# Kernel tuning notes

Hardware: AMD Instinct MI355X
Metric: run time of the kernel (lower is better)

The kernel has to match this reference:

```python
import jax, jax.numpy as jnp
import numpy as np

D_MODEL = 1024
BATCH = 4
SEQ = 4096


def setup_inputs() -> dict:
    key = jax.random.key(0)
    kx, kwz, kwh = jax.random.split(key, 3)
    scale = 1.0 / np.sqrt(D_MODEL)
    x = jax.random.normal(kx, (BATCH, SEQ, D_MODEL), dtype=jnp.float32)
    Wz = jax.random.normal(kwz, (D_MODEL, D_MODEL), dtype=jnp.float32) * scale
    bz = jnp.zeros((D_MODEL,), dtype=jnp.float32)
    Wh = jax.random.normal(kwh, (D_MODEL, D_MODEL), dtype=jnp.float32) * scale
    bh = jnp.zeros((D_MODEL,), dtype=jnp.float32)
    return {"x": x, "Wz": Wz, "bz": bz, "Wh": Wh, "bh": bh}


def _parallel_scan_real(a, b):
    # h_t = a_t * h_{t-1} + b_t via log-depth associative scan along time axis.
    def binary_op(left, right):
        a_l, b_l = left
        a_r, b_r = right
        return (a_l * a_r, a_r * b_l + b_r)
    _, h = jax.lax.associative_scan(binary_op, (a, b), axis=1)
    return h


def reference(x, Wz, bz, Wh, bh):
    # x: [B, T, D]
    z = jax.nn.sigmoid(jnp.einsum('btd,de->bte', x, Wz) + bz)  # update gate
    h_tilde = jnp.einsum('btd,de->bte', x, Wh) + bh            # candidate
    return _parallel_scan_real(1.0 - z, z * h_tilde)           # [B, T, D]
```

## Files before the change

kernel.cpp:

```cpp
#include <hip/hip_runtime.h>
#include <hip/hip_bf16.h>
#include <stdint.h>

#define D_MODEL 1024
#define BATCH   4
#define SEQ     4096
#define M_TOTAL (BATCH*SEQ)
#define KDIM    D_MODEL

#define NC 128
#define CL (SEQ/NC)

#define BM 128
#define BN 128
#define BK 32

typedef __bf16 bf16x8 __attribute__((ext_vector_type(8)));
typedef float  f32x4  __attribute__((ext_vector_type(4)));

static __device__ __forceinline__ unsigned short f2bf(float f) {
  unsigned u = __builtin_bit_cast(unsigned, f);
  u += 0x7FFFu + ((u >> 16) & 1u);
  return (unsigned short)(u >> 16);
}

__global__ __launch_bounds__(256) void k_cvt_x(const float* __restrict__ x,
                                               unsigned short* __restrict__ xb) {
  int i = blockIdx.x * 256 + threadIdx.x;
  float4 v = ((const float4*)x)[i];
  ushort4 o;
  o.x = f2bf(v.x); o.y = f2bf(v.y); o.z = f2bf(v.z); o.w = f2bf(v.w);
  ((ushort4*)xb)[i] = o;
}

__global__ void k_cvt_wT(const float* __restrict__ Wz, const float* __restrict__ Wh,
                         unsigned short* __restrict__ WzT, unsigned short* __restrict__ WhT) {
  __shared__ float tile[32][33];
  const float* W = blockIdx.z ? Wh : Wz;
  unsigned short* O = blockIdx.z ? WhT : WzT;
  int bx = blockIdx.x * 32;
  int by = blockIdx.y * 32;
  int tx = threadIdx.x, ty = threadIdx.y;
  for (int yy = ty; yy < 32; yy += 8)
    tile[yy][tx] = W[(size_t)(by + yy) * D_MODEL + bx + tx];
  __syncthreads();
  for (int yy = ty; yy < 32; yy += 8)
    O[(size_t)(bx + yy) * D_MODEL + by + tx] = f2bf(tile[tx][yy]);
}

__global__ __launch_bounds__(256) void k_gemm_dual(
    const unsigned short* __restrict__ xb,
    const unsigned short* __restrict__ WzT,
    const unsigned short* __restrict__ WhT,
    float* __restrict__ P, float* __restrict__ Q)
{
  __shared__ unsigned short As[BM * BK];
  __shared__ unsigned short Bs[BN * BK];
  const int tid  = threadIdx.x;
  const int wave = tid >> 6;
  const int lane = tid & 63;
  const int bm = blockIdx.x;
  const int bn = blockIdx.y;
  const unsigned short* Wt = (bn < 8) ? WzT : WhT;
  float* Cout = (bn < 8) ? P : Q;
  const int n0 = (bn & 7) * BN;
  const int m0 = bm * BM;

  const int wr = wave >> 1;
  const int wc = wave & 1;
  const int lr = lane & 15;
  const int lkB = (lane >> 4) * 16;

  f32x4 acc[4][4];
  #pragma unroll
  for (int i = 0; i < 4; ++i)
    #pragma unroll
    for (int j = 0; j < 4; ++j) acc[i][j] = (f32x4){0.f, 0.f, 0.f, 0.f};

  const int c0 = tid;
  const int c1 = tid + 256;
  const int r0 = c0 >> 2, kc0 = (c0 & 3) * 8;
  const int r1 = c1 >> 2, kc1 = (c1 & 3) * 8;

  for (int kt = 0; kt < KDIM; kt += BK) {
    const unsigned short* gA0 = xb + (size_t)(m0 + r0) * KDIM + kt + kc0;
    const unsigned short* gA1 = xb + (size_t)(m0 + r1) * KDIM + kt + kc1;
    const unsigned short* gB0 = Wt + (size_t)(n0 + r0) * KDIM + kt + kc0;
    const unsigned short* gB1 = Wt + (size_t)(n0 + r1) * KDIM + kt + kc1;
    __builtin_amdgcn_global_load_lds(
        (const __attribute__((address_space(1))) unsigned int*)gA0,
        (__attribute__((address_space(3))) unsigned int*)((char*)As + wave * 1024),
        16, 0, 0);
    __builtin_amdgcn_global_load_lds(
        (const __attribute__((address_space(1))) unsigned int*)gA1,
        (__attribute__((address_space(3))) unsigned int*)((char*)As + 4096 + wave * 1024),
        16, 0, 0);
    __builtin_amdgcn_global_load_lds(
        (const __attribute__((address_space(1))) unsigned int*)gB0,
        (__attribute__((address_space(3))) unsigned int*)((char*)Bs + wave * 1024),
        16, 0, 0);
    __builtin_amdgcn_global_load_lds(
        (const __attribute__((address_space(1))) unsigned int*)gB1,
        (__attribute__((address_space(3))) unsigned int*)((char*)Bs + 4096 + wave * 1024),
        16, 0, 0);
    __syncthreads();

    bf16x8 af[4], bfr[4];
    #pragma unroll
    for (int i = 0; i < 4; ++i)
      af[i] = *(const bf16x8*)((const char*)As + (wr*64 + i*16 + lr) * (BK*2) + lkB);
    #pragma unroll
    for (int j = 0; j < 4; ++j)
      bfr[j] = *(const bf16x8*)((const char*)Bs + (wc*64 + j*16 + lr) * (BK*2) + lkB);
    #pragma unroll
    for (int i = 0; i < 4; ++i)
      #pragma unroll
      for (int j = 0; j < 4; ++j)
        acc[i][j] = __builtin_amdgcn_mfma_f32_16x16x32_bf16(af[i], bfr[j], acc[i][j], 0, 0, 0);
    __syncthreads();
  }

  const int cb = lane & 15;
  const int rb = (lane >> 4) * 4;
  #pragma unroll
  for (int i = 0; i < 4; ++i) {
    #pragma unroll
    for (int j = 0; j < 4; ++j) {
      const size_t col = (size_t)(n0 + wc*64 + j*16 + cb);
      const size_t rowbase = (size_t)(m0 + wr*64 + i*16 + rb);
      #pragma unroll
      for (int r = 0; r < 4; ++r)
        Cout[(rowbase + r) * D_MODEL + col] = acc[i][j][r];
    }
  }
}

__global__ __launch_bounds__(256) void k_scan_agg(
    const float* __restrict__ P, const float* __restrict__ Q,
    const float* __restrict__ bz, const float* __restrict__ bh,
    float* __restrict__ Aagg, float* __restrict__ Bagg)
{
  int c = blockIdx.x & (NC - 1);
  int b = blockIdx.x >> 7;
  int d = threadIdx.x * 4;
  f32x4 vbz = *(const f32x4*)(bz + d);
  f32x4 vbh = *(const f32x4*)(bh + d);
  f32x4 A = {1.f, 1.f, 1.f, 1.f}, Bv = {0.f, 0.f, 0.f, 0.f};
  size_t base = ((size_t)b * SEQ + (size_t)c * CL) * D_MODEL + d;
  for (int t = 0; t < CL; ++t) {
    f32x4 p = *(const f32x4*)(P + base + (size_t)t * D_MODEL);
    f32x4 q = *(const f32x4*)(Q + base + (size_t)t * D_MODEL);
    #pragma unroll
    for (int r = 0; r < 4; ++r) {
      float z = 1.f / (1.f + __expf(-(p[r] + vbz[r])));
      float a = 1.f - z;
      float bb = z * (q[r] + vbh[r]);
      Bv[r] = a * Bv[r] + bb;
      A[r]  = a * A[r];
    }
  }
  size_t o = ((size_t)b * NC + c) * D_MODEL + d;
  *(f32x4*)(Aagg + o) = A;
  *(f32x4*)(Bagg + o) = Bv;
}

__global__ __launch_bounds__(256) void k_scan_chunks(
    const float* __restrict__ Aagg, const float* __restrict__ Bagg,
    float* __restrict__ Pref)
{
  int idx = blockIdx.x * 256 + threadIdx.x;
  int b = idx >> 10, d = idx & 1023;
  float h = 0.f;
  for (int cc = 0; cc < NC; ++cc) {
    size_t o = ((size_t)b * NC + cc) * D_MODEL + d;
    Pref[o] = h;
    h = Aagg[o] * h + Bagg[o];
  }
}

__global__ __launch_bounds__(256) void k_scan_apply(
    const float* __restrict__ P, float* __restrict__ Q,
    const float* __restrict__ bz, const float* __restrict__ bh,
    const float* __restrict__ Pref)
{
  int c = blockIdx.x & (NC - 1);
  int b = blockIdx.x >> 7;
  int d = threadIdx.x * 4;
  f32x4 vbz = *(const f32x4*)(bz + d);
  f32x4 vbh = *(const f32x4*)(bh + d);
  f32x4 h = *(const f32x4*)(Pref + ((size_t)b * NC + c) * D_MODEL + d);
  size_t base = ((size_t)b * SEQ + (size_t)c * CL) * D_MODEL + d;
  for (int t = 0; t < CL; ++t) {
    f32x4 p = *(const f32x4*)(P + base + (size_t)t * D_MODEL);
    f32x4 q = *(const f32x4*)(Q + base + (size_t)t * D_MODEL);
    #pragma unroll
    for (int r = 0; r < 4; ++r) {
      float z = 1.f / (1.f + __expf(-(p[r] + vbz[r])));
      float a = 1.f - z;
      h[r] = a * h[r] + z * (q[r] + vbh[r]);
    }
    *(f32x4*)(Q + base + (size_t)t * D_MODEL) = h;
  }
}

extern "C" void kernel_launch(void* const* d_in, const int* in_sizes, int n_in,
                              void* d_out, int out_size, void* d_ws, size_t ws_size,
                              hipStream_t stream)
{
  const float* x  = (const float*)d_in[0];
  const float* Wz = (const float*)d_in[1];
  const float* bz = (const float*)d_in[2];
  const float* Wh = (const float*)d_in[3];
  const float* bh = (const float*)d_in[4];

  char* ws = (char*)d_ws;
  unsigned short* xb  = (unsigned short*)(ws);
  unsigned short* WzT = (unsigned short*)(ws + 33554432);
  unsigned short* WhT = (unsigned short*)(ws + 35651584);
  float* P    = (float*)(ws + 37748736);
  float* Aagg = (float*)(ws + 104857600);
  float* Bagg = (float*)(ws + 106954752);
  float* Pref = (float*)(ws + 109051904);
  float* Q = (float*)d_out;

  k_cvt_x<<<M_TOTAL * D_MODEL / 4 / 256, 256, 0, stream>>>(x, xb);
  k_cvt_wT<<<dim3(32, 32, 2), dim3(32, 8), 0, stream>>>(Wz, Wh, WzT, WhT);
  k_gemm_dual<<<dim3(M_TOTAL / BM, 16), 256, 0, stream>>>(xb, WzT, WhT, P, Q);
  k_scan_agg<<<BATCH * NC, 256, 0, stream>>>(P, Q, bz, bh, Aagg, Bagg);
  k_scan_chunks<<<BATCH * D_MODEL / 256, 256, 0, stream>>>(Aagg, Bagg, Pref);
  k_scan_apply<<<BATCH * NC, 256, 0, stream>>>(P, Q, bz, bh, Pref);
}
```

Baseline: 192.7 us.

## Use 256x256 triple-buffered GEMM tiles and store gate pre-activations in bf16

Replaces the 128x128 dual GEMM with a 512-thread, 256x256-tile kernel. It treats both weight matrices as one concatenated N=2048 operand and triple-buffers LDS loads with explicit vmcnt waits and MFMA priority hints. GEMM outputs P and Q are now written as bf16 instead of fp32, which halves intermediate traffic for the GEMM store and both scan passes; the final scan writes to a separate fp32 output. This trades extra rounding of the pre-activations and higher register/LDS pressure for more data reuse and less memory bandwidth.

```diff
diff --git a/kernel.cpp b/kernel.cpp
--- a/kernel.cpp
+++ b/kernel.cpp
@@ -7,21 +7,27 @@
 #define SEQ     4096
 #define M_TOTAL (BATCH*SEQ)
 #define KDIM    D_MODEL
+#define NTOT    2048
 
 #define NC 128
 #define CL (SEQ/NC)
 
-#define BM 128
-#define BN 128
+#define BM 256
+#define BN 256
 #define BK 32
+#define NT (KDIM/BK)
 
 typedef __bf16 bf16x8 __attribute__((ext_vector_type(8)));
 typedef float  f32x4  __attribute__((ext_vector_type(4)));
+typedef unsigned short u16x4 __attribute__((ext_vector_type(4)));
 
 static __device__ __forceinline__ unsigned short f2bf(float f) {
   unsigned u = __builtin_bit_cast(unsigned, f);
   u += 0x7FFFu + ((u >> 16) & 1u);
   return (unsigned short)(u >> 16);
+}
+static __device__ __forceinline__ float bf2f(unsigned short u) {
+  return __builtin_bit_cast(float, (unsigned)u << 16);
 }
 
 __global__ __launch_bounds__(256) void k_cvt_x(const float* __restrict__ x,
@@ -48,95 +54,123 @@
     O[(size_t)(bx + yy) * D_MODEL + by + tx] = f2bf(tile[tx][yy]);
 }
 
-__global__ __launch_bounds__(256) void k_gemm_dual(
+__global__ __launch_bounds__(512, 2) void k_gemm8(
     const unsigned short* __restrict__ xb,
-    const unsigned short* __restrict__ WzT,
-    const unsigned short* __restrict__ WhT,
-    float* __restrict__ P, float* __restrict__ Q)
-{
-  __shared__ unsigned short As[BM * BK];
-  __shared__ unsigned short Bs[BN * BK];
+    const unsigned short* __restrict__ Wall,
+    unsigned short* __restrict__ P, unsigned short* __restrict__ Q)
+{
+  __shared__ __attribute__((aligned(16))) unsigned short lds[3 * 16384];
+
   const int tid  = threadIdx.x;
   const int wave = tid >> 6;
   const int lane = tid & 63;
-  const int bm = blockIdx.x;
-  const int bn = blockIdx.y;
-  const unsigned short* Wt = (bn < 8) ? WzT : WhT;
-  float* Cout = (bn < 8) ? P : Q;
-  const int n0 = (bn & 7) * BN;
-  const int m0 = bm * BM;
-
-  const int wr = wave >> 1;
-  const int wc = wave & 1;
+  const int m0 = blockIdx.x * BM;
+  const int n0 = blockIdx.y * BN;
+  const int wr = wave >> 2;
+  const int wc = wave & 3;
   const int lr = lane & 15;
-  const int lkB = (lane >> 4) * 16;
-
-  f32x4 acc[4][4];
+  const int lc = lane >> 4;
+
+  const int p0 = wave * 2, p1 = wave * 2 + 1;
+  const int c0 = p0 >> 2, rb0 = p0 & 3;
+  const int c1 = p1 >> 2, rb1 = p1 & 3;
+
+  f32x4 acc[8][4];
   #pragma unroll
-  for (int i = 0; i < 4; ++i)
+  for (int i = 0; i < 8; ++i)
     #pragma unroll
     for (int j = 0; j < 4; ++j) acc[i][j] = (f32x4){0.f, 0.f, 0.f, 0.f};
 
-  const int c0 = tid;
-  const int c1 = tid + 256;
-  const int r0 = c0 >> 2, kc0 = (c0 & 3) * 8;
-  const int r1 = c1 >> 2, kc1 = (c1 & 3) * 8;
-
-  for (int kt = 0; kt < KDIM; kt += BK) {
-    const unsigned short* gA0 = xb + (size_t)(m0 + r0) * KDIM + kt + kc0;
-    const unsigned short* gA1 = xb + (size_t)(m0 + r1) * KDIM + kt + kc1;
-    const unsigned short* gB0 = Wt + (size_t)(n0 + r0) * KDIM + kt + kc0;
-    const unsigned short* gB1 = Wt + (size_t)(n0 + r1) * KDIM + kt + kc1;
-    __builtin_amdgcn_global_load_lds(
-        (const __attribute__((address_space(1))) unsigned int*)gA0,
-        (__attribute__((address_space(3))) unsigned int*)((char*)As + wave * 1024),
-        16, 0, 0);
-    __builtin_amdgcn_global_load_lds(
-        (const __attribute__((address_space(1))) unsigned int*)gA1,
-        (__attribute__((address_space(3))) unsigned int*)((char*)As + 4096 + wave * 1024),
-        16, 0, 0);
-    __builtin_amdgcn_global_load_lds(
-        (const __attribute__((address_space(1))) unsigned int*)gB0,
-        (__attribute__((address_space(3))) unsigned int*)((char*)Bs + wave * 1024),
-        16, 0, 0);
-    __builtin_amdgcn_global_load_lds(
-        (const __attribute__((address_space(1))) unsigned int*)gB1,
-        (__attribute__((address_space(3))) unsigned int*)((char*)Bs + 4096 + wave * 1024),
-        16, 0, 0);
-    __syncthreads();
-
-    bf16x8 af[4], bfr[4];
-    #pragma unroll
-    for (int i = 0; i < 4; ++i)
-      af[i] = *(const bf16x8*)((const char*)As + (wr*64 + i*16 + lr) * (BK*2) + lkB);
-    #pragma unroll
-    for (int j = 0; j < 4; ++j)
-      bfr[j] = *(const bf16x8*)((const char*)Bs + (wc*64 + j*16 + lr) * (BK*2) + lkB);
-    #pragma unroll
-    for (int i = 0; i < 4; ++i)
+  auto stage = [&](int kt, int bufb) {
+    const int kb = kt * BK;
+    unsigned short* ldsA = &lds[bufb * 16384];
+    unsigned short* ldsB = ldsA + 8192;
+    const unsigned short* a0 = xb   + (size_t)(m0 + rb0*64 + lane) * KDIM + kb + c0*8;
+    const unsigned short* a1 = xb   + (size_t)(m0 + rb1*64 + lane) * KDIM + kb + c1*8;
+    const unsigned short* b0 = Wall + (size_t)(n0 + rb0*64 + lane) * KDIM + kb + c0*8;
+    const unsigned short* b1 = Wall + (size_t)(n0 + rb1*64 + lane) * KDIM + kb + c1*8;
+    __builtin_amdgcn_global_load_lds((const __attribute__((address_space(1))) unsigned int*)a0,
+        (__attribute__((address_space(3))) unsigned int*)(ldsA + (c0*256 + rb0*64)*8), 16, 0, 0);
+    __builtin_amdgcn_global_load_lds((const __attribute__((address_space(1))) unsigned int*)a1,
+        (__attribute__((address_space(3))) unsigned int*)(ldsA + (c1*256 + rb1*64)*8), 16, 0, 0);
+    __builtin_amdgcn_global_load_lds((const __attribute__((address_space(1))) unsigned int*)b0,
+        (__attribute__((address_space(3))) unsigned int*)(ldsB + (c0*256 + rb0*64)*8), 16, 0, 0);
+    __builtin_amdgcn_global_load_lds((const __attribute__((address_space(1))) unsigned int*)b1,
+        (__attribute__((address_space(3))) unsigned int*)(ldsB + (c1*256 + rb1*64)*8), 16, 0, 0);
+  };
+
+  stage(0, 0);
+  stage(1, 1);
+  asm volatile("s_waitcnt vmcnt(4)" ::: "memory");
+  __builtin_amdgcn_s_barrier();
+
+  const int aoff = (lc * 256 + wr * 128 + lr) * 8;
+  const int boff = (lc * 256 + wc * 64  + lr) * 8;
+
+  int buf = 0;
+  for (int kt = 0; kt < NT; ++kt) {
+    if (kt + 2 < NT) {
+      int db = buf + 2; if (db >= 3) db -= 3;
+      stage(kt + 2, db);
+    }
+
+    const unsigned short* bufA = &lds[buf * 16384];
+    const unsigned short* bufB = bufA + 8192;
+
+    bf16x8 bfrag[4];
+    #pragma unroll
+    for (int nf = 0; nf < 4; ++nf)
+      bfrag[nf] = *(const bf16x8*)(bufB + boff + nf * 128);
+    bf16x8 afrag[4];
+    #pragma unroll
+    for (int mf = 0; mf < 4; ++mf)
+      afrag[mf] = *(const bf16x8*)(bufA + aoff + mf * 128);
+
+    __builtin_amdgcn_s_setprio(1);
+    #pragma unroll
+    for (int mf = 0; mf < 4; ++mf)
       #pragma unroll
-      for (int j = 0; j < 4; ++j)
-        acc[i][j] = __builtin_amdgcn_mfma_f32_16x16x32_bf16(af[i], bfr[j], acc[i][j], 0, 0, 0);
-    __syncthreads();
-  }
-
+      for (int nf = 0; nf < 4; ++nf)
+        acc[mf][nf] = __builtin_amdgcn_mfma_f32_16x16x32_bf16(afrag[mf], bfrag[nf], acc[mf][nf], 0, 0, 0);
+    __builtin_amdgcn_s_setprio(0);
+
+    #pragma unroll
+    for (int mf = 0; mf < 4; ++mf)
+      afrag[mf] = *(const bf16x8*)(bufA + aoff + (mf + 4) * 128);
+
+    __builtin_amdgcn_s_setprio(1);
+    #pragma unroll
+    for (int mf = 0; mf < 4; ++mf)
+      #pragma unroll
+      for (int nf = 0; nf < 4; ++nf)
+        acc[mf + 4][nf] = __builtin_amdgcn_mfma_f32_16x16x32_bf16(afrag[mf], bfrag[nf], acc[mf + 4][nf], 0, 0, 0);
+    __builtin_amdgcn_s_setprio(0);
+
+    if (kt < NT - 2) asm volatile("s_waitcnt vmcnt(4)" ::: "memory");
+    else             asm volatile("s_waitcnt vmcnt(0)" ::: "memory");
+    __builtin_amdgcn_s_barrier();
+    buf = (buf == 2) ? 0 : buf + 1;
+  }
+
+  unsigned short* Cout = (n0 < 1024) ? P : Q;
+  const int colb = (n0 < 1024) ? n0 : (n0 - 1024);
   const int cb = lane & 15;
-  const int rb = (lane >> 4) * 4;
+  const int rb4 = (lane >> 4) * 4;
   #pragma unroll
-  for (int i = 0; i < 4; ++i) {
-    #pragma unroll
-    for (int j = 0; j < 4; ++j) {
-      const size_t col = (size_t)(n0 + wc*64 + j*16 + cb);
-      const size_t rowbase = (size_t)(m0 + wr*64 + i*16 + rb);
+  for (int mf = 0; mf < 8; ++mf) {
+    #pragma unroll
+    for (int nf = 0; nf < 4; ++nf) {
+      const size_t col  = (size_t)(colb + wc * 64 + nf * 16 + cb);
+      const size_t row0 = (size_t)(m0 + wr * 128 + mf * 16 + rb4);
       #pragma unroll
       for (int r = 0; r < 4; ++r)
-        Cout[(rowbase + r) * D_MODEL + col] = acc[i][j][r];
+        Cout[(row0 + r) * D_MODEL + col] = f2bf(acc[mf][nf][r]);
     }
   }
 }
 
 __global__ __launch_bounds__(256) void k_scan_agg(
-    const float* __restrict__ P, const float* __restrict__ Q,
+    const unsigned short* __restrict__ P, const unsigned short* __restrict__ Q,
     const float* __restrict__ bz, const float* __restrict__ bh,
     float* __restrict__ Aagg, float* __restrict__ Bagg)
 {
@@ -148,13 +182,13 @@
   f32x4 A = {1.f, 1.f, 1.f, 1.f}, Bv = {0.f, 0.f, 0.f, 0.f};
   size_t base = ((size_t)b * SEQ + (size_t)c * CL) * D_MODEL + d;
   for (int t = 0; t < CL; ++t) {
-    f32x4 p = *(const f32x4*)(P + base + (size_t)t * D_MODEL);
-    f32x4 q = *(const f32x4*)(Q + base + (size_t)t * D_MODEL);
+    u16x4 pu = *(const u16x4*)(P + base + (size_t)t * D_MODEL);
+    u16x4 qu = *(const u16x4*)(Q + base + (size_t)t * D_MODEL);
     #pragma unroll
     for (int r = 0; r < 4; ++r) {
-      float z = 1.f / (1.f + __expf(-(p[r] + vbz[r])));
+      float z = 1.f / (1.f + __expf(-(bf2f(pu[r]) + vbz[r])));
       float a = 1.f - z;
-      float bb = z * (q[r] + vbh[r]);
+      float bb = z * (bf2f(qu[r]) + vbh[r]);
       Bv[r] = a * Bv[r] + bb;
       A[r]  = a * A[r];
     }
@@ -179,9 +213,9 @@
 }
 
 __global__ __launch_bounds__(256) void k_scan_apply(
-    const float* __restrict__ P, float* __restrict__ Q,
+    const unsigned short* __restrict__ P, const unsigned short* __restrict__ Q,
     const float* __restrict__ bz, const float* __restrict__ bh,
-    const float* __restrict__ Pref)
+    const float* __restrict__ Pref, float* __restrict__ out)
 {
   int c = blockIdx.x & (NC - 1);
   int b = blockIdx.x >> 7;
@@ -191,15 +225,15 @@
   f32x4 h = *(const f32x4*)(Pref + ((size_t)b * NC + c) * D_MODEL + d);
   size_t base = ((size_t)b * SEQ + (size_t)c * CL) * D_MODEL + d;
   for (int t = 0; t < CL; ++t) {
-    f32x4 p = *(const f32x4*)(P + base + (size_t)t * D_MODEL);
-    f32x4 q = *(const f32x4*)(Q + base + (size_t)t * D_MODEL);
+    u16x4 pu = *(const u16x4*)(P + base + (size_t)t * D_MODEL);
+    u16x4 qu = *(const u16x4*)(Q + base + (size_t)t * D_MODEL);
     #pragma unroll
     for (int r = 0; r < 4; ++r) {
-      float z = 1.f / (1.f + __expf(-(p[r] + vbz[r])));
+      float z = 1.f / (1.f + __expf(-(bf2f(pu[r]) + vbz[r])));
       float a = 1.f - z;
-      h[r] = a * h[r] + z * (q[r] + vbh[r]);
-    }
-    *(f32x4*)(Q + base + (size_t)t * D_MODEL) = h;
+      h[r] = a * h[r] + z * (bf2f(qu[r]) + vbh[r]);
+    }
+    *(f32x4*)(out + base + (size_t)t * D_MODEL) = h;
   }
 }
 
@@ -214,19 +248,19 @@
   const float* bh = (const float*)d_in[4];
 
   char* ws = (char*)d_ws;
-  unsigned short* xb  = (unsigned short*)(ws);
-  unsigned short* WzT = (unsigned short*)(ws + 33554432);
-  unsigned short* WhT = (unsigned short*)(ws + 35651584);
-  float* P    = (float*)(ws + 37748736);
+  unsigned short* xb   = (unsigned short*)(ws);
+  unsigned short* Wall = (unsigned short*)(ws + 33554432);
+  unsigned short* Pb   = (unsigned short*)(ws + 37748736);
+  unsigned short* Qb   = (unsigned short*)(ws + 71303168);
   float* Aagg = (float*)(ws + 104857600);
   float* Bagg = (float*)(ws + 106954752);
   float* Pref = (float*)(ws + 109051904);
-  float* Q = (float*)d_out;
+  float* out  = (float*)d_out;
 
   k_cvt_x<<<M_TOTAL * D_MODEL / 4 / 256, 256, 0, stream>>>(x, xb);
-  k_cvt_wT<<<dim3(32, 32, 2), dim3(32, 8), 0, stream>>>(Wz, Wh, WzT, WhT);
-  k_gemm_dual<<<dim3(M_TOTAL / BM, 16), 256, 0, stream>>>(xb, WzT, WhT, P, Q);
-  k_scan_agg<<<BATCH * NC, 256, 0, stream>>>(P, Q, bz, bh, Aagg, Bagg);
+  k_cvt_wT<<<dim3(32, 32, 2), dim3(32, 8), 0, stream>>>(Wz, Wh, Wall, Wall + (size_t)1024 * 1024);
+  k_gemm8<<<dim3(M_TOTAL / BM, NTOT / BN), 512, 0, stream>>>(xb, Wall, Pb, Qb);
+  k_scan_agg<<<BATCH * NC, 256, 0, stream>>>(Pb, Qb, bz, bh, Aagg, Bagg);
   k_scan_chunks<<<BATCH * D_MODEL / 256, 256, 0, stream>>>(Aagg, Bagg, Pref);
-  k_scan_apply<<<BATCH * NC, 256, 0, stream>>>(P, Q, bz, bh, Pref);
-}
+  k_scan_apply<<<BATCH * NC, 256, 0, stream>>>(Pb, Qb, bz, bh, Pref, out);
+}
```

Result: faster. 162.4 us (-15.7%).
